# Kernel tuning notes

Hardware: AMD Instinct MI355X
Metric: run time of the kernel (lower is better)

The kernel has to match this reference:

```python
import jax, jax.numpy as jnp
import numpy as np

BB = 128  # CfC backbone_units default

def lecun_tanh(x):
    return 1.7159 * jnp.tanh(0.666 * x)

def cfc_scan(xs, Wb, bb, W1, b1, wtau, A):
    """CfC 'pure' mode RNN. xs: (N, T, Din) -> (N, T, H)."""
    H = A.shape[-1]
    h0 = jnp.zeros((xs.shape[0], H), xs.dtype)
    def step(h, x_t):
        z = jnp.concatenate([x_t, h], axis=-1)
        g = lecun_tanh(z @ Wb + bb)                       # backbone, 1 layer
        ff1 = g @ W1 + b1
        h_new = -A * jnp.exp(-(jnp.abs(wtau) + jnp.abs(ff1))) * ff1 + A
        return h_new, h_new
    _, ys = jax.lax.scan(step, h0, jnp.swapaxes(xs, 0, 1))
    return jnp.swapaxes(ys, 0, 1)

def ln2(x, g, b, eps=1e-8):
    """LayerNorm over last two dims (width, hidden)."""
    mu = jnp.mean(x, axis=(-2, -1), keepdims=True)
    var = jnp.mean((x - mu) ** 2, axis=(-2, -1), keepdims=True)
    return (x - mu) / jnp.sqrt(var + eps) * g + b

def setup_inputs() -> dict:
    key = jax.random.key(0)
    B, C, T, F = 8, 64, 250, 161
    H = 64
    Hh = H // 2  # intra hidden per direction
    ks = iter(jax.random.split(key, 40))
    def rn(shape, s=0.05):
        return jax.random.normal(next(ks), shape, dtype=jnp.float32) * s
    inp = {"x": jax.random.normal(next(ks), (B, C, T, F), dtype=jnp.float32)}
    def cell(prefix, din, h):
        inp[prefix + "_Wb"] = rn((din + h, BB))
        inp[prefix + "_bb"] = rn((BB,))
        inp[prefix + "_W1"] = rn((BB, h))
        inp[prefix + "_b1"] = rn((h,))
        inp[prefix + "_wtau"] = rn((h,))
        inp[prefix + "_A"] = 1.0 + rn((h,))
    cell("i1", C, Hh)   # intra forward
    cell("i2", C, Hh)   # intra backward
    cell("r", C, H)     # inter
    inp["intra_fc_W"] = rn((H, H)); inp["intra_fc_b"] = rn((H,))
    inp["intra_ln_g"] = 1.0 + rn((F, H)); inp["intra_ln_b"] = rn((F, H))
    inp["inter_fc_W"] = rn((H, H)); inp["inter_fc_b"] = rn((H,))
    inp["inter_ln_g"] = 1.0 + rn((F, H)); inp["inter_ln_b"] = rn((F, H))
    return inp

def reference(x, i1_Wb, i1_bb, i1_W1, i1_b1, i1_wtau, i1_A,
              i2_Wb, i2_bb, i2_W1, i2_b1, i2_wtau, i2_A,
              r_Wb, r_bb, r_W1, r_b1, r_wtau, r_A,
              intra_fc_W, intra_fc_b, intra_ln_g, intra_ln_b,
              inter_fc_W, inter_fc_b, inter_ln_g, inter_ln_b):
    B, C, T, F = x.shape
    H = inter_fc_b.shape[0]
    xp = jnp.transpose(x, (0, 2, 3, 1))                     # (B,T,F,C)
    # intra: bidirectional CfC over frequency axis
    intra_in = xp.reshape(B * T, F, C)
    y1 = cfc_scan(intra_in, i1_Wb, i1_bb, i1_W1, i1_b1, i1_wtau, i1_A)
    y2 = cfc_scan(intra_in[:, ::-1, :], i2_Wb, i2_bb, i2_W1, i2_b1, i2_wtau, i2_A)
    intra = jnp.concatenate([y1, y2], axis=-1)              # (B*T,F,H) -- note: reverse branch NOT flipped back (faithful)
    intra = intra @ intra_fc_W + intra_fc_b
    intra = intra.reshape(B, T, F, H)
    intra = ln2(intra, intra_ln_g, intra_ln_b)
    intra_out = xp + intra                                  # (B,T,F,H)
    # inter: unidirectional CfC over time axis
    xi = jnp.transpose(intra_out, (0, 2, 1, 3))             # (B,F,T,H)
    inter_in = xi.reshape(B * F, T, H)
    inter = cfc_scan(inter_in, r_Wb, r_bb, r_W1, r_b1, r_wtau, r_A)
    inter = inter @ inter_fc_W + inter_fc_b
    inter = inter.reshape(B, F, T, H)
    inter = jnp.transpose(inter, (0, 2, 1, 3))              # (B,T,F,H)
    inter = ln2(inter, inter_ln_g, inter_ln_b)
    inter_out = intra_out + inter
    return jnp.transpose(inter_out, (0, 3, 1, 2))           # (B,H,T,F)
```

## Files before the change

### kernel.cpp

```cpp
#include <hip/hip_runtime.h>
#include <cstdint>
#include <cstddef>

#define BBN 128
#define NBT 2000
#define NF  161
#define GROUP (NF * 64)

typedef __attribute__((ext_vector_type(4))) float f32x4;
typedef __attribute__((ext_vector_type(8))) __bf16 bf16x8;
typedef __attribute__((ext_vector_type(8))) uint16_t u16x8;

__device__ __forceinline__ uint16_t bf16_rne_u16(float f) {
  uint32_t u = __float_as_uint(f);
  return (uint16_t)((u + 0x7fffu + ((u >> 16) & 1u)) >> 16);
}
__device__ __forceinline__ float bf16u_to_f(uint16_t h) {
  return __uint_as_float((uint32_t)h << 16);
}
__device__ __forceinline__ float lecun_tanh_f(float x) {
  float e = __expf(1.332f * x);
  return 1.7159f * (1.f - __fdividef(2.f, e + 1.f));
}
__device__ __forceinline__ f32x4 mfma16(bf16x8 a, bf16x8 b, f32x4 c) {
  return __builtin_amdgcn_mfma_f32_16x16x32_bf16(a, b, c, 0, 0, 0);
}
__device__ __forceinline__ bf16x8 pack_frag(const float* __restrict__ base, int stride) {
  u16x8 t;
#pragma unroll
  for (int i = 0; i < 8; ++i) t[i] = bf16_rne_u16(base[i * stride]);
  return __builtin_bit_cast(bf16x8, t);
}

__device__ __forceinline__ void block_fence() {
  __builtin_amdgcn_sched_barrier(0);
  asm volatile("s_waitcnt lgkmcnt(0)" ::: "memory");
  __builtin_amdgcn_sched_barrier(0);
  __builtin_amdgcn_s_barrier();
  __builtin_amdgcn_sched_barrier(0);
}

__global__ __launch_bounds__(256) void transpose_kernel(
    const float* __restrict__ x, uint16_t* __restrict__ xph) {
  __shared__ float tile[32][33];
  const int bt = blockIdx.x;
  const int b = bt / 250, t = bt - b * 250;
  const int f0 = blockIdx.y * 32;
  const int c0 = blockIdx.z * 32;
  const int tx = threadIdx.x & 31;
  const int ty4 = (threadIdx.x >> 5) * 4;
  const int f_in = f0 + tx;
#pragma unroll
  for (int i = 0; i < 4; ++i) {
    int c = c0 + ty4 + i;
    if (f_in < NF)
      tile[ty4 + i][tx] = x[((size_t)(b * 64 + c) * 250 + t) * NF + f_in];
  }
  __syncthreads();
  const int c_out = c0 + tx;
#pragma unroll
  for (int i = 0; i < 4; ++i) {
    int f = f0 + ty4 + i;
    if (f < NF) {
      size_t o = ((size_t)bt * NF + f) * 64 + c_out;
      xph[o] = bf16_rne_u16(tile[tx][ty4 + i]);
    }
  }
}

template <int HD>
__global__ __launch_bounds__(512) void mfma_scan8(
    const uint16_t* __restrict__ in, uint16_t* __restrict__ out,
    const float* __restrict__ Wb0, const float* __restrict__ bb0,
    const float* __restrict__ W10, const float* __restrict__ b10,
    const float* __restrict__ wt0, const float* __restrict__ A0,
    const float* __restrict__ Wb1, const float* __restrict__ bb1,
    const float* __restrict__ W11, const float* __restrict__ b11,
    const float* __restrict__ wt1, const float* __restrict__ A1,
    int seq_len, int blocksPerDir, int nseq, int seqs_per_outer,
    int outer_stride, int inner_stride, int step_stride,
    int o_seq_stride, int o_step_stride, int o_col_per_dir) {
  constexpr int NKH = HD / 32;
  constexpr int NKZ = 2 + NKH;
  constexpr int NM = HD / 16;
  __shared__ __align__(16) uint16_t gfrag[4 * 64 * 8];
  __shared__ __align__(16) uint16_t hfrag[NKH * 64 * 8];

  const int dir = (blockIdx.x >= (unsigned)blocksPerDir) ? 1 : 0;
  const int bid = blockIdx.x - dir * blocksPerDir;
  const float* __restrict__ Wb = dir ? Wb1 : Wb0;
  const float* __restrict__ bb = dir ? bb1 : bb0;
  const float* __restrict__ W1 = dir ? W11 : W10;
  const float* __restrict__ b1 = dir ? b11 : b10;
  const float* __restrict__ wt = dir ? wt1 : wt0;
  const float* __restrict__ Aa = dir ? A1 : A0;
  const bool rev = (dir == 1);
  const int tid = threadIdx.x;
  const int w = tid >> 6, l = tid & 63, l4 = l >> 4, lm = l & 15;
  const bool has_m = (w < NM);

  bf16x8 WB[NKZ];
  const float bbv = bb[16 * w + lm];
#pragma unroll
  for (int kt = 0; kt < NKZ; ++kt)
    WB[kt] = pack_frag(&Wb[(kt * 32 + l4 * 8) * BBN + 16 * w + lm], BBN);
  bf16x8 W1f[4];
  float b1v = 0.f, wtv = 0.f, Avv = 0.f;
  if (has_m) {
#pragma unroll
    for (int kt = 0; kt < 4; ++kt)
      W1f[kt] = pack_frag(&W1[(kt * 32 + l4 * 8) * HD + 16 * w + lm], HD);
    b1v = b1[16 * w + lm];
    wtv = fabsf(wt[16 * w + lm]);
    Avv = Aa[16 * w + lm];
  }

  int sA = bid * 16 + lm;
  if (sA > nseq - 1) sA = nseq - 1;
  int ob = sA / seqs_per_outer, oi = sA - ob * seqs_per_outer;
  const uint16_t* inp =
      in + (size_t)ob * outer_stride + (size_t)oi * inner_stride + l4 * 8;
  int obase[4];
  bool omask[4];
#pragma unroll
  for (int r = 0; r < 4; ++r) {
    int s = bid * 16 + l4 * 4 + r;
    omask[r] = has_m && (s < nseq);
    if (s > nseq - 1) s = nseq - 1;
    obase[r] = s * o_seq_stride + dir * o_col_per_dir + 16 * w + lm;
  }

  const int gi =
      ((w >> 1) * 64 + (2 * (w & 1) + (lm >> 3)) * 16 + l4 * 4) * 8 + (lm & 7);

  for (int e = tid; e < NKH * 64 * 8; e += 512) hfrag[e] = 0;
  block_fence();

  bf16x8 xa, xb;
  {
    int f0 = rev ? (seq_len - 1) : 0;
    xa = *(const bf16x8*)(inp + (size_t)f0 * step_stride);
    xb = *(const bf16x8*)(inp + (size_t)f0 * step_stride + 32);
  }

  for (int st = 0; st < seq_len; ++st) {
    bf16x8 hf[NKH];
#pragma unroll
    for (int kt = 0; kt < NKH; ++kt)
      hf[kt] = *(const bf16x8*)&hfrag[(kt * 64 + l) * 8];
    bf16x8 nxa = xa, nxb = xb;
    if (st + 1 < seq_len) {
      int f = rev ? (seq_len - 2 - st) : (st + 1);
      nxa = *(const bf16x8*)(inp + (size_t)f * step_stride);
      nxb = *(const bf16x8*)(inp + (size_t)f * step_stride + 32);
    }
    f32x4 a0 = {bbv, bbv, bbv, bbv};
    f32x4 a1 = {0.f, 0.f, 0.f, 0.f};
    a0 = mfma16(xa, WB[0], a0);
    a1 = mfma16(xb, WB[1], a1);
    a0 = mfma16(hf[0], WB[2], a0);
    if constexpr (NKH == 2) a1 = mfma16(hf[1], WB[3], a1);
    f32x4 acc = a0 + a1;
#pragma unroll
    for (int r = 0; r < 4; ++r)
      gfrag[gi + r * 8] = bf16_rne_u16(lecun_tanh_f(acc[r]));
    block_fence();

    if (has_m) {
      bf16x8 gf[4];
#pragma unroll
      for (int kt = 0; kt < 4; ++kt)
        gf[kt] = *(const bf16x8*)&gfrag[(kt * 64 + l) * 8];
      f32x4 f0 = {b1v, b1v, b1v, b1v};
      f32x4 f1 = {0.f, 0.f, 0.f, 0.f};
      f0 = mfma16(gf[0], W1f[0], f0);
      f1 = mfma16(gf[1], W1f[1], f1);
      f0 = mfma16(gf[2], W1f[2], f0);
      f1 = mfma16(gf[3], W1f[3], f1);
      f32x4 fa = f0 + f1;
#pragma unroll
      for (int r = 0; r < 4; ++r) {
        float ff = fa[r];
        float e = __expf(-(wtv + fabsf(ff)));
        float hn = fmaf(-Avv * e, ff, Avv);
        uint16_t hb = bf16_rne_u16(hn);
        hfrag[gi + r * 8] = hb;
        if (omask[r]) out[obase[r] + st * o_step_stride] = hb;
      }
    }
    block_fence();
    xa = nxa;
    xb = nxb;
  }
}

template <bool TRANS>
__global__ __launch_bounds__(256) void fc_ln_mfma(
    const uint16_t* __restrict__ yin, const uint16_t* __restrict__ resid,
    const float* __restrict__ W, const float* __restrict__ bias,
    const float* __restrict__ lng, const float* __restrict__ lnb,
    void* __restrict__ outp) {
  __shared__ __align__(16) uint16_t ysh[176 * 72];
  __shared__ float red[16];
  __shared__ float fsh[TRANS ? NF * 73 : 4];

  const int tid = threadIdx.x, n = blockIdx.x;
  const int w = tid >> 6, l = tid & 63, l4 = l >> 4, lm = l & 15;
  const int b = n / 250, t = n - b * 250;

  const size_t ybase = TRANS ? ((size_t)b * 40250 + t) * 64 : (size_t)n * GROUP;
  const int rstride = TRANS ? 16000 : 64;
  for (int idx = tid; idx < 176 * 8; idx += 256) {
    int f = idx >> 3, k8 = (idx & 7) * 8;
    uint64_t lo = 0, hi = 0;
    if (f < NF) {
      const uint64_t* p =
          (const uint64_t*)(yin + ybase + (size_t)f * rstride + k8);
      lo = p[0];
      hi = p[1];
    }
    uint64_t* q = (uint64_t*)&ysh[f * 72 + k8];
    q[0] = lo;
    q[1] = hi;
  }

  bf16x8 Wf[2];
#pragma unroll
  for (int kt = 0; kt < 2; ++kt)
    Wf[kt] = pack_frag(&W[(kt * 32 + l4 * 8) * 64 + 16 * w + lm], 64);
  const float bv = bias[16 * w + lm];
  __syncthreads();

  f32x4 acc[11];
#pragma unroll
  for (int m = 0; m < 11; ++m) {
    bf16x8 a0 = *(const bf16x8*)&ysh[(m * 16 + lm) * 72 + l4 * 8];
    bf16x8 a1 = *(const bf16x8*)&ysh[(m * 16 + lm) * 72 + 32 + l4 * 8];
    f32x4 c = {bv, bv, bv, bv};
    c = mfma16(a0, Wf[0], c);
    c = mfma16(a1, Wf[1], c);
    acc[m] = c;
  }

  float sum = 0.f, ssq = 0.f;
#pragma unroll
  for (int m = 0; m < 10; ++m)
#pragma unroll
    for (int r = 0; r < 4; ++r) {
      float v = acc[m][r];
      sum += v;
      ssq += v * v;
    }
  if (l4 == 0) {
    float v = acc[10][0];
    sum += v;
    ssq += v * v;
  }
#pragma unroll
  for (int off = 32; off; off >>= 1) {
    sum += __shfl_xor(sum, off);
    ssq += __shfl_xor(ssq, off);
  }
  if (l == 0) {
    red[w] = sum;
    red[4 + w] = ssq;
  }
  __syncthreads();
  if (tid == 0) {
    float s = red[0] + red[1] + red[2] + red[3];
    float q = red[4] + red[5] + red[6] + red[7];
    float mu = s * (1.f / (float)GROUP);
    float var = q * (1.f / (float)GROUP) - mu * mu;
    red[8] = mu;
    red[9] = rsqrtf(fmaxf(var, 0.f) + 1e-8f);
  }
  __syncthreads();
  const float mu = red[8], rstd = red[9];

#pragma unroll
  for (int m = 0; m < 11; ++m)
#pragma unroll
    for (int r = 0; r < 4; ++r) {
      int row = m * 16 + l4 * 4 + r;
      if (row < NF)
        ysh[row * 72 + 16 * w + lm] = bf16_rne_u16((acc[m][r] - mu) * rstd);
    }
  __syncthreads();

  const uint16_t* rrow = resid + (size_t)n * GROUP;
  if (!TRANS) {
    uint16_t* orow = (uint16_t*)outp + (size_t)n * GROUP;
    for (int idx = tid; idx < GROUP; idx += 256) {
      int f = idx >> 6, h = idx & 63;
      float v = bf16u_to_f(ysh[f * 72 + h]) * lng[idx] + lnb[idx] +
                bf16u_to_f(rrow[idx]);
      orow[idx] = bf16_rne_u16(v);
    }
  } else {
    for (int idx = tid; idx < GROUP; idx += 256) {
      int f = idx >> 6, h = idx & 63;
      fsh[f * 73 + h] = bf16u_to_f(ysh[f * 72 + h]) * lng[idx] + lnb[idx] +
                        bf16u_to_f(rrow[idx]);
    }
    __syncthreads();
    float* ob2 = (float*)outp + (size_t)b * 2576000 + (size_t)t * 161;
    for (int idx = tid; idx < GROUP; idx += 256) {
      unsigned h = (unsigned)idx / 161u, f = (unsigned)idx - h * 161u;
      ob2[(size_t)h * 40250 + f] = fsh[f * 73 + h];
    }
  }
}

extern "C" void kernel_launch(void* const* d_in, const int* in_sizes, int n_in,
                              void* d_out, int out_size, void* d_ws,
                              size_t ws_size, hipStream_t stream) {
  const float* x     = (const float*)d_in[0];
  const float* i1_Wb = (const float*)d_in[1];
  const float* i1_bb = (const float*)d_in[2];
  const float* i1_W1 = (const float*)d_in[3];
  const float* i1_b1 = (const float*)d_in[4];
  const float* i1_wt = (const float*)d_in[5];
  const float* i1_A  = (const float*)d_in[6];
  const float* i2_Wb = (const float*)d_in[7];
  const float* i2_bb = (const float*)d_in[8];
  const float* i2_W1 = (const float*)d_in[9];
  const float* i2_b1 = (const float*)d_in[10];
  const float* i2_wt = (const float*)d_in[11];
  const float* i2_A  = (const float*)d_in[12];
  const float* r_Wb  = (const float*)d_in[13];
  const float* r_bb  = (const float*)d_in[14];
  const float* r_W1  = (const float*)d_in[15];
  const float* r_b1  = (const float*)d_in[16];
  const float* r_wt  = (const float*)d_in[17];
  const float* r_A   = (const float*)d_in[18];
  const float* fcW_i = (const float*)d_in[19];
  const float* fcb_i = (const float*)d_in[20];
  const float* lng_i = (const float*)d_in[21];
  const float* lnb_i = (const float*)d_in[22];
  const float* fcW_r = (const float*)d_in[23];
  const float* fcb_r = (const float*)d_in[24];
  const float* lng_r = (const float*)d_in[25];
  const float* lnb_r = (const float*)d_in[26];

  uint8_t* ws = (uint8_t*)d_ws;
  uint16_t* xp_h    = (uint16_t*)ws;
  uint16_t* intra_h = (uint16_t*)(ws + 41216000);
  uint16_t* inter_h = (uint16_t*)(ws + 82432000);
  uint16_t* ybuf    = (uint16_t*)d_out;

  transpose_kernel<<<dim3(NBT, 6, 2), 256, 0, stream>>>(x, xp_h);

  mfma_scan8<32><<<250, 512, 0, stream>>>(
      xp_h, ybuf, i1_Wb, i1_bb, i1_W1, i1_b1, i1_wt, i1_A, i2_Wb, i2_bb, i2_W1,
      i2_b1, i2_wt, i2_A, 161, 125, 2000, 2000, 0, GROUP, 64, GROUP, 64, 32);

  fc_ln_mfma<false><<<NBT, 256, 0, stream>>>(ybuf, xp_h, fcW_i, fcb_i, lng_i,
                                             lnb_i, intra_h);

  mfma_scan8<64><<<81, 512, 0, stream>>>(
      intra_h, inter_h, r_Wb, r_bb, r_W1, r_b1, r_wt, r_A, r_Wb, r_bb, r_W1,
      r_b1, r_wt, r_A, 250, 81, 1288, 161, 250 * GROUP, 64, GROUP, 16000, 64,
      0);

  fc_ln_mfma<true><<<NBT, 256, 0, stream>>>(inter_h, intra_h, fcW_r, fcb_r,
                                            lng_r, lnb_r, d_out);
}
```

Measured before the change: 617.9 us.

## Shorten scan critical path with hoisted input MFMAs, raw exp/rcp, packed bf16 converts

In the recurrent scan, the input-projection MFMAs for the next step are issued right after the barrier, overlapping the W1 phase and leaving only the hidden-state MFMAs on the serial path. Activation math now uses raw v_exp_f32/v_rcp_f32 with pre-folded log2 constants, and bf16 packing uses v_cvt_pk_bf16_f32 in place of manual rounding. Sched barriers around the block fence are removed so the compiler can reorder more freely. The FC/LN epilogue is also vectorized to two elements per thread. Raw exp/rcp may differ slightly in precision and in edge-case handling from the library intrinsics.

```diff
diff --git a/kernel.cpp b/kernel.cpp
--- a/kernel.cpp
+++ b/kernel.cpp
@@ -18,9 +18,24 @@
 __device__ __forceinline__ float bf16u_to_f(uint16_t h) {
   return __uint_as_float((uint32_t)h << 16);
 }
+__device__ __forceinline__ uint32_t cvt_pk_bf16(float lo, float hi) {
+  uint32_t r;
+  asm("v_cvt_pk_bf16_f32 %0, %1, %2" : "=v"(r) : "v"(lo), "v"(hi));
+  return r;
+}
+__device__ __forceinline__ float asm_exp2(float x) {
+  float r;
+  asm("v_exp_f32 %0, %1" : "=v"(r) : "v"(x));
+  return r;
+}
+__device__ __forceinline__ float asm_rcp(float x) {
+  float r;
+  asm("v_rcp_f32 %0, %1" : "=v"(r) : "v"(x));
+  return r;
+}
 __device__ __forceinline__ float lecun_tanh_f(float x) {
-  float e = __expf(1.332f * x);
-  return 1.7159f * (1.f - __fdividef(2.f, e + 1.f));
+  float t = asm_exp2(1.9216698f * x);
+  return fmaf(asm_rcp(t + 1.f), -3.4318f, 1.7159f);
 }
 __device__ __forceinline__ f32x4 mfma16(bf16x8 a, bf16x8 b, f32x4 c) {
   return __builtin_amdgcn_mfma_f32_16x16x32_bf16(a, b, c, 0, 0, 0);
@@ -33,11 +48,8 @@
 }
 
 __device__ __forceinline__ void block_fence() {
-  __builtin_amdgcn_sched_barrier(0);
   asm volatile("s_waitcnt lgkmcnt(0)" ::: "memory");
-  __builtin_amdgcn_sched_barrier(0);
   __builtin_amdgcn_s_barrier();
-  __builtin_amdgcn_sched_barrier(0);
 }
 
 __global__ __launch_bounds__(256) void transpose_kernel(
@@ -81,7 +93,6 @@
     int outer_stride, int inner_stride, int step_stride,
     int o_seq_stride, int o_step_stride, int o_col_per_dir) {
   constexpr int NKH = HD / 32;
-  constexpr int NKZ = 2 + NKH;
   constexpr int NM = HD / 16;
   __shared__ __align__(16) uint16_t gfrag[4 * 64 * 8];
   __shared__ __align__(16) uint16_t hfrag[NKH * 64 * 8];
@@ -99,20 +110,25 @@
   const int w = tid >> 6, l = tid & 63, l4 = l >> 4, lm = l & 15;
   const bool has_m = (w < NM);
 
-  bf16x8 WB[NKZ];
+  bf16x8 WB[2 + NKH];
+#pragma unroll
+  for (int kt = 0; kt < 2 + NKH; ++kt)
+    WB[kt] = pack_frag(&Wb[(kt * 32 + l4 * 8) * BBN + 16 * w + lm], BBN);
   const float bbv = bb[16 * w + lm];
-#pragma unroll
-  for (int kt = 0; kt < NKZ; ++kt)
-    WB[kt] = pack_frag(&Wb[(kt * 32 + l4 * 8) * BBN + 16 * w + lm], BBN);
+  const f32x4 bbv4 = {bbv, bbv, bbv, bbv};
+  const f32x4 zero4 = {0.f, 0.f, 0.f, 0.f};
   bf16x8 W1f[4];
-  float b1v = 0.f, wtv = 0.f, Avv = 0.f;
+  f32x4 b1v4 = zero4;
+  float mwt2 = 0.f, nAv = 0.f, Avv = 0.f;
   if (has_m) {
 #pragma unroll
     for (int kt = 0; kt < 4; ++kt)
       W1f[kt] = pack_frag(&W1[(kt * 32 + l4 * 8) * HD + 16 * w + lm], HD);
-    b1v = b1[16 * w + lm];
-    wtv = fabsf(wt[16 * w + lm]);
+    float b1v = b1[16 * w + lm];
+    b1v4 = {b1v, b1v, b1v, b1v};
+    mwt2 = -1.4426950408889634f * fabsf(wt[16 * w + lm]);
     Avv = Aa[16 * w + lm];
+    nAv = -Avv;
   }
 
   int sA = bid * 16 + lm;
@@ -136,61 +152,72 @@
   for (int e = tid; e < NKH * 64 * 8; e += 512) hfrag[e] = 0;
   block_fence();
 
-  bf16x8 xa, xb;
+  bf16x8 nxa, nxb;
   {
     int f0 = rev ? (seq_len - 1) : 0;
-    xa = *(const bf16x8*)(inp + (size_t)f0 * step_stride);
-    xb = *(const bf16x8*)(inp + (size_t)f0 * step_stride + 32);
-  }
+    nxa = *(const bf16x8*)(inp + (size_t)f0 * step_stride);
+    nxb = *(const bf16x8*)(inp + (size_t)f0 * step_stride + 32);
+  }
+  f32x4 a0 = mfma16(nxa, WB[0], bbv4);
+  f32x4 a1 = mfma16(nxb, WB[1], zero4);
 
   for (int st = 0; st < seq_len; ++st) {
-    bf16x8 hf[NKH];
-#pragma unroll
-    for (int kt = 0; kt < NKH; ++kt)
-      hf[kt] = *(const bf16x8*)&hfrag[(kt * 64 + l) * 8];
-    bf16x8 nxa = xa, nxb = xb;
     if (st + 1 < seq_len) {
       int f = rev ? (seq_len - 2 - st) : (st + 1);
       nxa = *(const bf16x8*)(inp + (size_t)f * step_stride);
       nxb = *(const bf16x8*)(inp + (size_t)f * step_stride + 32);
     }
-    f32x4 a0 = {bbv, bbv, bbv, bbv};
-    f32x4 a1 = {0.f, 0.f, 0.f, 0.f};
-    a0 = mfma16(xa, WB[0], a0);
-    a1 = mfma16(xb, WB[1], a1);
-    a0 = mfma16(hf[0], WB[2], a0);
-    if constexpr (NKH == 2) a1 = mfma16(hf[1], WB[3], a1);
+    {
+      bf16x8 h0 = *(const bf16x8*)&hfrag[l * 8];
+      a0 = mfma16(h0, WB[2], a0);
+      if constexpr (NKH == 2) {
+        bf16x8 h1 = *(const bf16x8*)&hfrag[(64 + l) * 8];
+        a1 = mfma16(h1, WB[3], a1);
+      }
+    }
     f32x4 acc = a0 + a1;
-#pragma unroll
-    for (int r = 0; r < 4; ++r)
-      gfrag[gi + r * 8] = bf16_rne_u16(lecun_tanh_f(acc[r]));
+    {
+      uint32_t p01 = cvt_pk_bf16(lecun_tanh_f(acc[0]), lecun_tanh_f(acc[1]));
+      uint32_t p23 = cvt_pk_bf16(lecun_tanh_f(acc[2]), lecun_tanh_f(acc[3]));
+      gfrag[gi] = (uint16_t)p01;
+      gfrag[gi + 8] = (uint16_t)(p01 >> 16);
+      gfrag[gi + 16] = (uint16_t)p23;
+      gfrag[gi + 24] = (uint16_t)(p23 >> 16);
+    }
     block_fence();
 
+    a0 = mfma16(nxa, WB[0], bbv4);
+    a1 = mfma16(nxb, WB[1], zero4);
     if (has_m) {
       bf16x8 gf[4];
 #pragma unroll
       for (int kt = 0; kt < 4; ++kt)
         gf[kt] = *(const bf16x8*)&gfrag[(kt * 64 + l) * 8];
-      f32x4 f0 = {b1v, b1v, b1v, b1v};
-      f32x4 f1 = {0.f, 0.f, 0.f, 0.f};
-      f0 = mfma16(gf[0], W1f[0], f0);
-      f1 = mfma16(gf[1], W1f[1], f1);
+      f32x4 f0 = mfma16(gf[0], W1f[0], b1v4);
+      f32x4 f1 = mfma16(gf[1], W1f[1], zero4);
       f0 = mfma16(gf[2], W1f[2], f0);
       f1 = mfma16(gf[3], W1f[3], f1);
       f32x4 fa = f0 + f1;
+      float hn[4];
 #pragma unroll
       for (int r = 0; r < 4; ++r) {
         float ff = fa[r];
-        float e = __expf(-(wtv + fabsf(ff)));
-        float hn = fmaf(-Avv * e, ff, Avv);
-        uint16_t hb = bf16_rne_u16(hn);
-        hfrag[gi + r * 8] = hb;
-        if (omask[r]) out[obase[r] + st * o_step_stride] = hb;
+        float e = asm_exp2(fmaf(-1.4426950408889634f, fabsf(ff), mwt2));
+        hn[r] = fmaf(e * ff, nAv, Avv);
       }
+      uint32_t p01 = cvt_pk_bf16(hn[0], hn[1]);
+      uint32_t p23 = cvt_pk_bf16(hn[2], hn[3]);
+      uint16_t hb[4] = {(uint16_t)p01, (uint16_t)(p01 >> 16), (uint16_t)p23,
+                        (uint16_t)(p23 >> 16)};
+      hfrag[gi] = hb[0];
+      hfrag[gi + 8] = hb[1];
+      hfrag[gi + 16] = hb[2];
+      hfrag[gi + 24] = hb[3];
+#pragma unroll
+      for (int r = 0; r < 4; ++r)
+        if (omask[r]) out[obase[r] + st * o_step_stride] = hb[r];
     }
     block_fence();
-    xa = nxa;
-    xb = nxb;
   }
 }
 
@@ -290,17 +317,31 @@
   const uint16_t* rrow = resid + (size_t)n * GROUP;
   if (!TRANS) {
     uint16_t* orow = (uint16_t*)outp + (size_t)n * GROUP;
-    for (int idx = tid; idx < GROUP; idx += 256) {
-      int f = idx >> 6, h = idx & 63;
-      float v = bf16u_to_f(ysh[f * 72 + h]) * lng[idx] + lnb[idx] +
-                bf16u_to_f(rrow[idx]);
-      orow[idx] = bf16_rne_u16(v);
+    for (int i2 = tid; i2 < GROUP / 2; i2 += 256) {
+      int e0 = 2 * i2;
+      int f = e0 >> 6, h = e0 & 63;
+      float2 lg = *(const float2*)&lng[e0];
+      float2 lb = *(const float2*)&lnb[e0];
+      uint32_t rr = *(const uint32_t*)&rrow[e0];
+      uint32_t yv = *(const uint32_t*)&ysh[f * 72 + h];
+      float v0 = bf16u_to_f((uint16_t)yv) * lg.x + lb.x +
+                 bf16u_to_f((uint16_t)rr);
+      float v1 = bf16u_to_f((uint16_t)(yv >> 16)) * lg.y + lb.y +
+                 bf16u_to_f((uint16_t)(rr >> 16));
+      *(uint32_t*)&orow[e0] = cvt_pk_bf16(v0, v1);
     }
   } else {
-    for (int idx = tid; idx < GROUP; idx += 256) {
-      int f = idx >> 6, h = idx & 63;
-      fsh[f * 73 + h] = bf16u_to_f(ysh[f * 72 + h]) * lng[idx] + lnb[idx] +
-                        bf16u_to_f(rrow[idx]);
+    for (int i2 = tid; i2 < GROUP / 2; i2 += 256) {
+      int e0 = 2 * i2;
+      int f = e0 >> 6, h = e0 & 63;
+      float2 lg = *(const float2*)&lng[e0];
+      float2 lb = *(const float2*)&lnb[e0];
+      uint32_t rr = *(const uint32_t*)&rrow[e0];
+      uint32_t yv = *(const uint32_t*)&ysh[f * 72 + h];
+      fsh[f * 73 + h] = bf16u_to_f((uint16_t)yv) * lg.x + lb.x +
+                        bf16u_to_f((uint16_t)rr);
+      fsh[f * 73 + h + 1] = bf16u_to_f((uint16_t)(yv >> 16)) * lg.y + lb.y +
+                            bf16u_to_f((uint16_t)(rr >> 16));
     }
     __syncthreads();
     float* ob2 = (float*)outp + (size_t)b * 2576000 + (size_t)t * 161;
```

After: 708.6 us. 1.15x slower.
